# Kernel optimization log

Measured on AMD Instinct MI355X. Metric: run time of the kernel, lower is better.

The kernel has to match this reference:

```python
import jax, jax.numpy as jnp
import numpy as np

ALPHA = 0.2  # LeakyReLU negative slope
NEG = -9e15


def gat_layer(h, adj, W, a):
    # Faithful to the torch GAT: e_ij = leakyrelu(a^T [Wh_i || Wh_j])
    # = leakyrelu(a_src . Wh_i + a_dst . Wh_j); avoids the NxNx2F materialization.
    Wh = h @ W                              # [N, F]
    Fo = W.shape[1]
    a_src, a_dst = a[:Fo, 0], a[Fo:, 0]
    e = jax.nn.leaky_relu(
        (Wh @ a_src)[:, None] + (Wh @ a_dst)[None, :], negative_slope=ALPHA
    )                                        # [N, N]
    e = jnp.where(adj > 0, e, NEG)
    att = jax.nn.softmax(e, axis=1)          # dropout p=0 (eval)
    return jax.nn.elu(att @ Wh)


def gru_cell(x, h, W_ih, W_hh, b_ih, b_hh):
    # PyTorch GRUCell semantics.
    gi = x @ W_ih.T + b_ih                   # [N, 3F]
    gh = h @ W_hh.T + b_hh
    i_r, i_z, i_n = jnp.split(gi, 3, axis=1)
    h_r, h_z, h_n = jnp.split(gh, 3, axis=1)
    r = jax.nn.sigmoid(i_r + h_r)
    z = jax.nn.sigmoid(i_z + h_z)
    n = jnp.tanh(i_n + r * h_n)
    return (1.0 - z) * n + z * h


def setup_inputs() -> dict:
    key = jax.random.key(0)
    ks = jax.random.split(key, 10)
    N, nfeat, nhid, nout = 8192, 256, 128, 128
    x = jax.random.normal(ks[0], (N, nfeat), dtype=jnp.float32)
    # sparse random binary adjacency (~32 avg degree) + self loops
    adj = (jax.random.uniform(ks[1], (N, N)) < 0.004).astype(jnp.float32)
    adj = jnp.maximum(adj, jnp.eye(N, dtype=jnp.float32))
    h_prev = jnp.zeros((N, nout), dtype=jnp.float32)

    def xavier(k, shape, gain=1.414):
        fan_in, fan_out = shape[0], shape[1]
        b = gain * np.sqrt(6.0 / (fan_in + fan_out))
        return jax.random.uniform(k, shape, jnp.float32, -b, b)

    W1 = xavier(ks[2], (nfeat, nhid))
    a1 = xavier(ks[3], (2 * nhid, 1))
    W2 = xavier(ks[4], (nhid, nout))
    a2 = xavier(ks[5], (2 * nout, 1))
    s = 1.0 / np.sqrt(nout)
    W_ih = jax.random.uniform(ks[6], (3 * nout, nout), jnp.float32, -s, s)
    W_hh = jax.random.uniform(ks[7], (3 * nout, nout), jnp.float32, -s, s)
    b_ih = jax.random.uniform(ks[8], (3 * nout,), jnp.float32, -s, s)
    b_hh = jax.random.uniform(ks[9], (3 * nout,), jnp.float32, -s, s)
    return {"x": x, "adj": adj, "h_prev": h_prev, "W1": W1, "a1": a1,
            "W2": W2, "a2": a2, "W_ih": W_ih, "W_hh": W_hh,
            "b_ih": b_ih, "b_hh": b_hh}


def reference(x, adj, h_prev, W1, a1, W2, a2, W_ih, W_hh, b_ih, b_hh):
    x1 = gat_layer(x, adj, W1, a1)
    h_spat = gat_layer(x1, adj, W2, a2)
    return gru_cell(h_spat, h_prev, W_ih, W_hh, b_ih, b_hh)
```

## Files before the change

### kernel.cpp

```cpp
#include <hip/hip_runtime.h>
#include <math.h>

#define N_NODES 8192
#define CAP 128
#define LRELU_ALPHA 0.2f

typedef float v4f __attribute__((ext_vector_type(4)));

template <int K>
__device__ __forceinline__ void gemm_srcdst_body(
    int r0, int t, const float* __restrict__ A, const float* __restrict__ W,
    const float* __restrict__ a, float* __restrict__ Wh, float* __restrict__ src,
    float* __restrict__ dst, float* As, float (*red)[4][2]) {
  int c = t & 127, half = t >> 7;
  const float4* Ab4 = (const float4*)(A + (size_t)r0 * K);
  float4* As4 = (float4*)As;
#pragma unroll
  for (int l = t; l < 8 * K / 4; l += 256) As4[l] = Ab4[l];
  __syncthreads();
  float acc[4] = {0.f, 0.f, 0.f, 0.f};
  const float* Asl = As + (half * 4) * K;
#pragma unroll 8
  for (int k = 0; k < K; k++) {
    float wv = W[k * 128 + c];
#pragma unroll
    for (int r = 0; r < 4; r++) acc[r] += Asl[r * K + k] * wv;
  }
  float as = a[c], ad = a[128 + c];
  int wv_id = t >> 6, lane = t & 63;
#pragma unroll
  for (int r = 0; r < 4; r++) {
    int row = half * 4 + r;
    Wh[(size_t)(r0 + row) * 128 + c] = acc[r];
    float s = acc[r] * as, d = acc[r] * ad;
#pragma unroll
    for (int off = 32; off; off >>= 1) {
      s += __shfl_xor(s, off);
      d += __shfl_xor(d, off);
    }
    if (lane == 0) { red[wv_id][r][0] = s; red[wv_id][r][1] = d; }
  }
  __syncthreads();
  if (t < 8) {
    int wa = (t < 4) ? 0 : 2, rr = t & 3;
    src[r0 + t] = red[wa][rr][0] + red[wa + 1][rr][0];
    dst[r0 + t] = red[wa][rr][1] + red[wa + 1][rr][1];
  }
}

#define TR_B 64
__global__ __launch_bounds__(256) void gemm1_kernel(
    const float* __restrict__ x, const float* __restrict__ W1, const float* __restrict__ a1,
    float* __restrict__ Wh1, float* __restrict__ src1, float* __restrict__ dst1,
    const float* __restrict__ Wi, const float* __restrict__ Whm, float* __restrict__ WiT,
    float* __restrict__ WhT) {
  __shared__ float As[8 * 256];
  __shared__ float red[4][4][2];
  int t = threadIdx.x, bid = blockIdx.x;
  if (bid < 1024) {
    gemm_srcdst_body<256>(bid * 8, t, x, W1, a1, Wh1, src1, dst1, As, red);
  } else {
    for (int n = (bid - 1024) * 256 + t; n < 384 * 128; n += TR_B * 256) {
      int r = n >> 7, c = n & 127;
      WiT[c * 384 + r] = Wi[n];
      WhT[c * 384 + r] = Whm[n];
    }
  }
}

__global__ __launch_bounds__(256) void scan_agg_kernel(
    const float* __restrict__ adj, const float* __restrict__ Wh, const float* __restrict__ src,
    const float* __restrict__ dst, int* __restrict__ idx, int* __restrict__ counts,
    float* __restrict__ outp) {
  __shared__ int jn[CAP];
  __shared__ float w[CAP];
  __shared__ float redm[4];
  __shared__ float reds[4];
  __shared__ float accs[128];
  __shared__ int cnt;
  int i = blockIdx.x, t = threadIdx.x, lane = t & 63, wv = t >> 6;
  if (t == 0) cnt = 0;
  __syncthreads();
  const v4f* row = (const v4f*)(adj + (size_t)i * N_NODES);
  v4f v[8];
#pragma unroll
  for (int u = 0; u < 8; u++) v[u] = __builtin_nontemporal_load(row + t + 256 * u);
#pragma unroll
  for (int u = 0; u < 8; u++) {
    int n = (v[u].x > 0.f) + (v[u].y > 0.f) + (v[u].z > 0.f) + (v[u].w > 0.f);
    if (n) {
      int p = atomicAdd(&cnt, n);
      int j0 = (t + 256 * u) * 4;
      if (v[u].x > 0.f) { if (p < CAP) jn[p] = j0;     p++; }
      if (v[u].y > 0.f) { if (p < CAP) jn[p] = j0 + 1; p++; }
      if (v[u].z > 0.f) { if (p < CAP) jn[p] = j0 + 2; p++; }
      if (v[u].w > 0.f) { if (p < CAP) jn[p] = j0 + 3; p++; }
    }
  }
  __syncthreads();
  int c = cnt > CAP ? CAP : cnt;
  if (t < c) idx[(size_t)i * CAP + t] = jn[t];
  if (t == 0) counts[i] = c;
  float si = src[i];
  float e = -1e30f;
  if (t < c) {
    float x = si + dst[jn[t]];
    e = x > 0.f ? x : LRELU_ALPHA * x;
  }
  float m = e;
#pragma unroll
  for (int off = 32; off; off >>= 1) m = fmaxf(m, __shfl_xor(m, off));
  if (lane == 0) redm[wv] = m;
  __syncthreads();
  float M = fmaxf(fmaxf(redm[0], redm[1]), fmaxf(redm[2], redm[3]));
  float ex = 0.f;
  if (t < c) {
    ex = expf(e - M);
    w[t] = ex;
  }
  float s = ex;
#pragma unroll
  for (int off = 32; off; off >>= 1) s += __shfl_xor(s, off);
  if (lane == 0) reds[wv] = s;
  __syncthreads();
  float inv = 1.f / (reds[0] + reds[1] + reds[2] + reds[3]);
  int col = t & 127, half = t >> 7;
  float acc = 0.f;
  int k = half;
  for (; k + 2 < c; k += 4) {
    acc += w[k] * Wh[(size_t)jn[k] * 128 + col] + w[k + 2] * Wh[(size_t)jn[k + 2] * 128 + col];
  }
  for (; k < c; k += 2) acc += w[k] * Wh[(size_t)jn[k] * 128 + col];
  if (half == 0) accs[col] = acc;
  __syncthreads();
  if (half == 1) {
    float a = (accs[col] + acc) * inv;
    outp[(size_t)i * 128 + col] = a > 0.f ? a : expf(a) - 1.f;
  }
}

__global__ __launch_bounds__(256) void agg2_kernel(
    const float* __restrict__ Wh, const float* __restrict__ src, const float* __restrict__ dst,
    const int* __restrict__ idx, const int* __restrict__ counts, float* __restrict__ outp) {
  __shared__ int jn[CAP];
  __shared__ float w[CAP];
  __shared__ float redm[4];
  __shared__ float reds[4];
  __shared__ float accs[128];
  int i = blockIdx.x, t = threadIdx.x, lane = t & 63, wv = t >> 6;
  int c = counts[i];
  float si = src[i];
  float e = -1e30f;
  if (t < c) {
    int j = idx[(size_t)i * CAP + t];
    jn[t] = j;
    float x = si + dst[j];
    e = x > 0.f ? x : LRELU_ALPHA * x;
  }
  float m = e;
#pragma unroll
  for (int off = 32; off; off >>= 1) m = fmaxf(m, __shfl_xor(m, off));
  if (lane == 0) redm[wv] = m;
  __syncthreads();
  float M = fmaxf(fmaxf(redm[0], redm[1]), fmaxf(redm[2], redm[3]));
  float ex = 0.f;
  if (t < c) {
    ex = expf(e - M);
    w[t] = ex;
  }
  float s = ex;
#pragma unroll
  for (int off = 32; off; off >>= 1) s += __shfl_xor(s, off);
  if (lane == 0) reds[wv] = s;
  __syncthreads();
  float inv = 1.f / (reds[0] + reds[1] + reds[2] + reds[3]);
  int col = t & 127, half = t >> 7;
  float acc = 0.f;
  int k = half;
  for (; k + 2 < c; k += 4) {
    acc += w[k] * Wh[(size_t)jn[k] * 128 + col] + w[k + 2] * Wh[(size_t)jn[k + 2] * 128 + col];
  }
  for (; k < c; k += 2) acc += w[k] * Wh[(size_t)jn[k] * 128 + col];
  if (half == 0) accs[col] = acc;
  __syncthreads();
  if (half == 1) {
    float a = (accs[col] + acc) * inv;
    outp[(size_t)i * 128 + col] = a > 0.f ? a : expf(a) - 1.f;
  }
}

__global__ __launch_bounds__(256) void gemm_srcdst2_kernel(
    const float* __restrict__ A, const float* __restrict__ W, const float* __restrict__ a,
    float* __restrict__ Wh, float* __restrict__ src, float* __restrict__ dst) {
  __shared__ float As[8 * 128];
  __shared__ float red[4][4][2];
  gemm_srcdst_body<128>(blockIdx.x * 8, threadIdx.x, A, W, a, Wh, src, dst, As, red);
}

__global__ __launch_bounds__(256) void gru_kernel(
    const float* __restrict__ x, const float* __restrict__ h, const float* __restrict__ WiT,
    const float* __restrict__ WhT, const float* __restrict__ b_ih,
    const float* __restrict__ b_hh, float* __restrict__ outp) {
  __shared__ float xs[8 * 128];
  __shared__ float hs[8 * 128];
  int t = threadIdx.x, c = t & 127, half = t >> 7;
  int r0 = blockIdx.x * 8;
  {
    const float4* xb = (const float4*)(x + (size_t)r0 * 128);
    const float4* hb = (const float4*)(h + (size_t)r0 * 128);
    ((float4*)xs)[t] = xb[t];
    ((float4*)hs)[t] = hb[t];
  }
  __syncthreads();
  const float* xsl = xs + half * 4 * 128;
  const float* hsl = hs + half * 4 * 128;
  float rg[4], zg[4];
  {
    float ai[4] = {0.f}, ah[4] = {0.f};
#pragma unroll 4
    for (int k = 0; k < 128; k++) {
      float wi = WiT[k * 384 + c];
      float wh = WhT[k * 384 + c];
#pragma unroll
      for (int r = 0; r < 4; r++) {
        ai[r] += xsl[r * 128 + k] * wi;
        ah[r] += hsl[r * 128 + k] * wh;
      }
    }
    float bi = b_ih[c], bh = b_hh[c];
#pragma unroll
    for (int r = 0; r < 4; r++) rg[r] = 1.f / (1.f + expf(-(ai[r] + bi + ah[r] + bh)));
  }
  {
    float ai[4] = {0.f}, ah[4] = {0.f};
#pragma unroll 4
    for (int k = 0; k < 128; k++) {
      float wi = WiT[k * 384 + 128 + c];
      float wh = WhT[k * 384 + 128 + c];
#pragma unroll
      for (int r = 0; r < 4; r++) {
        ai[r] += xsl[r * 128 + k] * wi;
        ah[r] += hsl[r * 128 + k] * wh;
      }
    }
    float bi = b_ih[128 + c], bh = b_hh[128 + c];
#pragma unroll
    for (int r = 0; r < 4; r++) zg[r] = 1.f / (1.f + expf(-(ai[r] + bi + ah[r] + bh)));
  }
  {
    float ai[4] = {0.f}, ah[4] = {0.f};
#pragma unroll 4
    for (int k = 0; k < 128; k++) {
      float wi = WiT[k * 384 + 256 + c];
      float wh = WhT[k * 384 + 256 + c];
#pragma unroll
      for (int r = 0; r < 4; r++) {
        ai[r] += xsl[r * 128 + k] * wi;
        ah[r] += hsl[r * 128 + k] * wh;
      }
    }
    float bi = b_ih[256 + c], bh = b_hh[256 + c];
#pragma unroll
    for (int r = 0; r < 4; r++) {
      float n = tanhf(ai[r] + bi + rg[r] * (ah[r] + bh));
      float o = (1.f - zg[r]) * n + zg[r] * hsl[r * 128 + c];
      outp[(size_t)(r0 + half * 4 + r) * 128 + c] = o;
    }
  }
}

extern "C" void kernel_launch(void* const* d_in, const int* in_sizes, int n_in,
                              void* d_out, int out_size, void* d_ws, size_t ws_size,
                              hipStream_t stream) {
  const float* x     = (const float*)d_in[0];
  const float* adj   = (const float*)d_in[1];
  const float* hprev = (const float*)d_in[2];
  const float* W1    = (const float*)d_in[3];
  const float* a1    = (const float*)d_in[4];
  const float* W2    = (const float*)d_in[5];
  const float* a2    = (const float*)d_in[6];
  const float* W_ih  = (const float*)d_in[7];
  const float* W_hh  = (const float*)d_in[8];
  const float* b_ih  = (const float*)d_in[9];
  const float* b_hh  = (const float*)d_in[10];
  float* outp = (float*)d_out;

  char* p = (char*)d_ws;
  float* Wh1    = (float*)p; p += (size_t)N_NODES * 128 * 4;
  float* Wh2    = (float*)p; p += (size_t)N_NODES * 128 * 4;
  float* x1     = (float*)p; p += (size_t)N_NODES * 128 * 4;
  float* h_spat = (float*)p; p += (size_t)N_NODES * 128 * 4;
  float* src1   = (float*)p; p += (size_t)N_NODES * 4;
  float* dst1   = (float*)p; p += (size_t)N_NODES * 4;
  float* src2   = (float*)p; p += (size_t)N_NODES * 4;
  float* dst2   = (float*)p; p += (size_t)N_NODES * 4;
  float* WiT    = (float*)p; p += (size_t)384 * 128 * 4;
  float* WhT    = (float*)p; p += (size_t)384 * 128 * 4;
  int*   counts = (int*)p;   p += (size_t)N_NODES * 4;
  int*   idxbuf = (int*)p;   p += (size_t)N_NODES * CAP * 4;

  gemm1_kernel<<<1024 + TR_B, 256, 0, stream>>>(x, W1, a1, Wh1, src1, dst1, W_ih, W_hh, WiT, WhT);
  scan_agg_kernel<<<N_NODES, 256, 0, stream>>>(adj, Wh1, src1, dst1, idxbuf, counts, x1);
  gemm_srcdst2_kernel<<<N_NODES / 8, 256, 0, stream>>>(x1, W2, a2, Wh2, src2, dst2);
  agg2_kernel<<<N_NODES, 256, 0, stream>>>(Wh2, src2, dst2, idxbuf, counts, h_spat);
  gru_kernel<<<N_NODES / 8, 256, 0, stream>>>(h_spat, hprev, WiT, WhT, b_ih, b_hh, outp);
}
```

Baseline: 512.9 us.

## Fuse all stages into one cooperative persistent kernel with grid syncs

Replaces five separate launches with a single cooperative persistent kernel that runs every stage in grid-stride loops separated by grid.sync. Odd blocks scan adjacency rows first while even blocks run the first GEMM first, so the memory-bound adjacency scan overlaps with compute. Splitting the scan from the first aggregation means the gathered neighbour indices are written to and then reread from global memory. The change removes launch gaps and tail effects, but adds grid-wide barriers and limits the grid to resident occupancy, which can reduce latency hiding in the gather-heavy phases.

```diff
diff --git a/kernel.cpp b/kernel.cpp
--- a/kernel.cpp
+++ b/kernel.cpp
@@ -1,5 +1,8 @@
 #include <hip/hip_runtime.h>
+#include <hip/hip_cooperative_groups.h>
 #include <math.h>
+
+namespace cg = cooperative_groups;
 
 #define N_NODES 8192
 #define CAP 128
@@ -46,40 +49,13 @@
     src[r0 + t] = red[wa][rr][0] + red[wa + 1][rr][0];
     dst[r0 + t] = red[wa][rr][1] + red[wa + 1][rr][1];
   }
-}
-
-#define TR_B 64
-__global__ __launch_bounds__(256) void gemm1_kernel(
-    const float* __restrict__ x, const float* __restrict__ W1, const float* __restrict__ a1,
-    float* __restrict__ Wh1, float* __restrict__ src1, float* __restrict__ dst1,
-    const float* __restrict__ Wi, const float* __restrict__ Whm, float* __restrict__ WiT,
-    float* __restrict__ WhT) {
-  __shared__ float As[8 * 256];
-  __shared__ float red[4][4][2];
-  int t = threadIdx.x, bid = blockIdx.x;
-  if (bid < 1024) {
-    gemm_srcdst_body<256>(bid * 8, t, x, W1, a1, Wh1, src1, dst1, As, red);
-  } else {
-    for (int n = (bid - 1024) * 256 + t; n < 384 * 128; n += TR_B * 256) {
-      int r = n >> 7, c = n & 127;
-      WiT[c * 384 + r] = Wi[n];
-      WhT[c * 384 + r] = Whm[n];
-    }
-  }
-}
-
-__global__ __launch_bounds__(256) void scan_agg_kernel(
-    const float* __restrict__ adj, const float* __restrict__ Wh, const float* __restrict__ src,
-    const float* __restrict__ dst, int* __restrict__ idx, int* __restrict__ counts,
-    float* __restrict__ outp) {
-  __shared__ int jn[CAP];
-  __shared__ float w[CAP];
-  __shared__ float redm[4];
-  __shared__ float reds[4];
-  __shared__ float accs[128];
-  __shared__ int cnt;
-  int i = blockIdx.x, t = threadIdx.x, lane = t & 63, wv = t >> 6;
-  if (t == 0) cnt = 0;
+  __syncthreads();
+}
+
+__device__ __forceinline__ void scan_row(int i, int t, const float* __restrict__ adj,
+                                         int* __restrict__ idxbuf, int* __restrict__ counts,
+                                         int* jn, int* cntp) {
+  if (t == 0) *cntp = 0;
   __syncthreads();
   const v4f* row = (const v4f*)(adj + (size_t)i * N_NODES);
   v4f v[8];
@@ -89,7 +65,7 @@
   for (int u = 0; u < 8; u++) {
     int n = (v[u].x > 0.f) + (v[u].y > 0.f) + (v[u].z > 0.f) + (v[u].w > 0.f);
     if (n) {
-      int p = atomicAdd(&cnt, n);
+      int p = atomicAdd(cntp, n);
       int j0 = (t + 256 * u) * 4;
       if (v[u].x > 0.f) { if (p < CAP) jn[p] = j0;     p++; }
       if (v[u].y > 0.f) { if (p < CAP) jn[p] = j0 + 1; p++; }
@@ -98,13 +74,28 @@
     }
   }
   __syncthreads();
-  int c = cnt > CAP ? CAP : cnt;
-  if (t < c) idx[(size_t)i * CAP + t] = jn[t];
+  int c = *cntp;
+  if (c > CAP) c = CAP;
+  if (t < c) idxbuf[(size_t)i * CAP + t] = jn[t];
   if (t == 0) counts[i] = c;
+  __syncthreads();
+}
+
+__device__ __forceinline__ void agg_body(int i, int t, const float* __restrict__ Wh,
+                                         const float* __restrict__ src,
+                                         const float* __restrict__ dst,
+                                         const int* __restrict__ idxbuf,
+                                         const int* __restrict__ counts,
+                                         float* __restrict__ outp, int* jn, float* w,
+                                         float* redm, float* reds, float* accs) {
+  int lane = t & 63, wv = t >> 6;
+  int c = counts[i];
   float si = src[i];
   float e = -1e30f;
   if (t < c) {
-    float x = si + dst[jn[t]];
+    int j = idxbuf[(size_t)i * CAP + t];
+    jn[t] = j;
+    float x = si + dst[j];
     e = x > 0.f ? x : LRELU_ALPHA * x;
   }
   float m = e;
@@ -127,9 +118,8 @@
   int col = t & 127, half = t >> 7;
   float acc = 0.f;
   int k = half;
-  for (; k + 2 < c; k += 4) {
+  for (; k + 2 < c; k += 4)
     acc += w[k] * Wh[(size_t)jn[k] * 128 + col] + w[k + 2] * Wh[(size_t)jn[k + 2] * 128 + col];
-  }
   for (; k < c; k += 2) acc += w[k] * Wh[(size_t)jn[k] * 128 + col];
   if (half == 0) accs[col] = acc;
   __syncthreads();
@@ -137,80 +127,19 @@
     float a = (accs[col] + acc) * inv;
     outp[(size_t)i * 128 + col] = a > 0.f ? a : expf(a) - 1.f;
   }
-}
-
-__global__ __launch_bounds__(256) void agg2_kernel(
-    const float* __restrict__ Wh, const float* __restrict__ src, const float* __restrict__ dst,
-    const int* __restrict__ idx, const int* __restrict__ counts, float* __restrict__ outp) {
-  __shared__ int jn[CAP];
-  __shared__ float w[CAP];
-  __shared__ float redm[4];
-  __shared__ float reds[4];
-  __shared__ float accs[128];
-  int i = blockIdx.x, t = threadIdx.x, lane = t & 63, wv = t >> 6;
-  int c = counts[i];
-  float si = src[i];
-  float e = -1e30f;
-  if (t < c) {
-    int j = idx[(size_t)i * CAP + t];
-    jn[t] = j;
-    float x = si + dst[j];
-    e = x > 0.f ? x : LRELU_ALPHA * x;
-  }
-  float m = e;
-#pragma unroll
-  for (int off = 32; off; off >>= 1) m = fmaxf(m, __shfl_xor(m, off));
-  if (lane == 0) redm[wv] = m;
-  __syncthreads();
-  float M = fmaxf(fmaxf(redm[0], redm[1]), fmaxf(redm[2], redm[3]));
-  float ex = 0.f;
-  if (t < c) {
-    ex = expf(e - M);
-    w[t] = ex;
-  }
-  float s = ex;
-#pragma unroll
-  for (int off = 32; off; off >>= 1) s += __shfl_xor(s, off);
-  if (lane == 0) reds[wv] = s;
-  __syncthreads();
-  float inv = 1.f / (reds[0] + reds[1] + reds[2] + reds[3]);
-  int col = t & 127, half = t >> 7;
-  float acc = 0.f;
-  int k = half;
-  for (; k + 2 < c; k += 4) {
-    acc += w[k] * Wh[(size_t)jn[k] * 128 + col] + w[k + 2] * Wh[(size_t)jn[k + 2] * 128 + col];
-  }
-  for (; k < c; k += 2) acc += w[k] * Wh[(size_t)jn[k] * 128 + col];
-  if (half == 0) accs[col] = acc;
-  __syncthreads();
-  if (half == 1) {
-    float a = (accs[col] + acc) * inv;
-    outp[(size_t)i * 128 + col] = a > 0.f ? a : expf(a) - 1.f;
-  }
-}
-
-__global__ __launch_bounds__(256) void gemm_srcdst2_kernel(
-    const float* __restrict__ A, const float* __restrict__ W, const float* __restrict__ a,
-    float* __restrict__ Wh, float* __restrict__ src, float* __restrict__ dst) {
-  __shared__ float As[8 * 128];
-  __shared__ float red[4][4][2];
-  gemm_srcdst_body<128>(blockIdx.x * 8, threadIdx.x, A, W, a, Wh, src, dst, As, red);
-}
-
-__global__ __launch_bounds__(256) void gru_kernel(
-    const float* __restrict__ x, const float* __restrict__ h, const float* __restrict__ WiT,
-    const float* __restrict__ WhT, const float* __restrict__ b_ih,
-    const float* __restrict__ b_hh, float* __restrict__ outp) {
-  __shared__ float xs[8 * 128];
-  __shared__ float hs[8 * 128];
-  int t = threadIdx.x, c = t & 127, half = t >> 7;
-  int r0 = blockIdx.x * 8;
-  {
-    const float4* xb = (const float4*)(x + (size_t)r0 * 128);
-    const float4* hb = (const float4*)(h + (size_t)r0 * 128);
-    ((float4*)xs)[t] = xb[t];
-    ((float4*)hs)[t] = hb[t];
-  }
+  __syncthreads();
+}
+
+__device__ __forceinline__ void gru_body(int r0, int t, const float* __restrict__ x,
+                                         const float* __restrict__ h,
+                                         const float* __restrict__ WiT,
+                                         const float* __restrict__ WhT,
+                                         const float* __restrict__ b_ih,
+                                         const float* __restrict__ b_hh,
+                                         float* __restrict__ outp, float* xs, float* hs) {
+  int c = t & 127, half = t >> 7;
+  ((float4*)xs)[t] = ((const float4*)(x + (size_t)r0 * 128))[t];
+  ((float4*)hs)[t] = ((const float4*)(h + (size_t)r0 * 128))[t];
   __syncthreads();
   const float* xsl = xs + half * 4 * 128;
   const float* hsl = hs + half * 4 * 128;
@@ -219,13 +148,9 @@
     float ai[4] = {0.f}, ah[4] = {0.f};
 #pragma unroll 4
     for (int k = 0; k < 128; k++) {
-      float wi = WiT[k * 384 + c];
-      float wh = WhT[k * 384 + c];
-#pragma unroll
-      for (int r = 0; r < 4; r++) {
-        ai[r] += xsl[r * 128 + k] * wi;
-        ah[r] += hsl[r * 128 + k] * wh;
-      }
+      float wi = WiT[k * 384 + c], wh = WhT[k * 384 + c];
+#pragma unroll
+      for (int r = 0; r < 4; r++) { ai[r] += xsl[r * 128 + k] * wi; ah[r] += hsl[r * 128 + k] * wh; }
     }
     float bi = b_ih[c], bh = b_hh[c];
 #pragma unroll
@@ -235,13 +160,9 @@
     float ai[4] = {0.f}, ah[4] = {0.f};
 #pragma unroll 4
     for (int k = 0; k < 128; k++) {
-      float wi = WiT[k * 384 + 128 + c];
-      float wh = WhT[k * 384 + 128 + c];
-#pragma unroll
-      for (int r = 0; r < 4; r++) {
-        ai[r] += xsl[r * 128 + k] * wi;
-        ah[r] += hsl[r * 128 + k] * wh;
-      }
+      float wi = WiT[k * 384 + 128 + c], wh = WhT[k * 384 + 128 + c];
+#pragma unroll
+      for (int r = 0; r < 4; r++) { ai[r] += xsl[r * 128 + k] * wi; ah[r] += hsl[r * 128 + k] * wh; }
     }
     float bi = b_ih[128 + c], bh = b_hh[128 + c];
 #pragma unroll
@@ -251,22 +172,80 @@
     float ai[4] = {0.f}, ah[4] = {0.f};
 #pragma unroll 4
     for (int k = 0; k < 128; k++) {
-      float wi = WiT[k * 384 + 256 + c];
-      float wh = WhT[k * 384 + 256 + c];
-#pragma unroll
-      for (int r = 0; r < 4; r++) {
-        ai[r] += xsl[r * 128 + k] * wi;
-        ah[r] += hsl[r * 128 + k] * wh;
-      }
+      float wi = WiT[k * 384 + 256 + c], wh = WhT[k * 384 + 256 + c];
+#pragma unroll
+      for (int r = 0; r < 4; r++) { ai[r] += xsl[r * 128 + k] * wi; ah[r] += hsl[r * 128 + k] * wh; }
     }
     float bi = b_ih[256 + c], bh = b_hh[256 + c];
 #pragma unroll
     for (int r = 0; r < 4; r++) {
       float n = tanhf(ai[r] + bi + rg[r] * (ah[r] + bh));
-      float o = (1.f - zg[r]) * n + zg[r] * hsl[r * 128 + c];
-      outp[(size_t)(r0 + half * 4 + r) * 128 + c] = o;
-    }
-  }
+      outp[(size_t)(r0 + half * 4 + r) * 128 + c] =
+          (1.f - zg[r]) * n + zg[r] * hsl[r * 128 + c];
+    }
+  }
+  __syncthreads();
+}
+
+__global__ __launch_bounds__(256, 4) void mega_kernel(
+    const float* __restrict__ x, const float* __restrict__ adj, const float* __restrict__ hprev,
+    const float* __restrict__ W1, const float* __restrict__ a1, const float* __restrict__ W2,
+    const float* __restrict__ a2, const float* __restrict__ Wi, const float* __restrict__ Whm,
+    const float* __restrict__ b_ih, const float* __restrict__ b_hh, float* __restrict__ outp,
+    float* __restrict__ Wh1, float* __restrict__ Wh2, float* __restrict__ x1,
+    float* __restrict__ h_spat, float* __restrict__ src1, float* __restrict__ dst1,
+    float* __restrict__ src2, float* __restrict__ dst2, float* __restrict__ WiT,
+    float* __restrict__ WhT, int* __restrict__ counts, int* __restrict__ idxbuf, int NB) {
+  cg::grid_group grid = cg::this_grid();
+  __shared__ float As[8 * 256];
+  __shared__ float red[4][4][2];
+  __shared__ int jn[CAP];
+  __shared__ float w[CAP];
+  __shared__ float redm[4];
+  __shared__ float reds[4];
+  __shared__ float accs[128];
+  __shared__ int cnt;
+  int b = blockIdx.x, t = threadIdx.x;
+
+  if (b & 1) {
+    for (int i = b; i < N_NODES; i += NB) scan_row(i, t, adj, idxbuf, counts, jn, &cnt);
+    for (int n = b * 256 + t; n < 384 * 128; n += NB * 256) {
+      int r = n >> 7, c = n & 127;
+      WiT[c * 384 + r] = Wi[n];
+      WhT[c * 384 + r] = Whm[n];
+    }
+    for (int tile = b; tile < 1024; tile += NB)
+      gemm_srcdst_body<256>(tile * 8, t, x, W1, a1, Wh1, src1, dst1, As, red);
+  } else {
+    for (int n = b * 256 + t; n < 384 * 128; n += NB * 256) {
+      int r = n >> 7, c = n & 127;
+      WiT[c * 384 + r] = Wi[n];
+      WhT[c * 384 + r] = Whm[n];
+    }
+    for (int tile = b; tile < 1024; tile += NB)
+      gemm_srcdst_body<256>(tile * 8, t, x, W1, a1, Wh1, src1, dst1, As, red);
+    for (int i = b; i < N_NODES; i += NB) scan_row(i, t, adj, idxbuf, counts, jn, &cnt);
+  }
+  __threadfence();
+  grid.sync();
+
+  for (int i = b; i < N_NODES; i += NB)
+    agg_body(i, t, Wh1, src1, dst1, idxbuf, counts, x1, jn, w, redm, reds, accs);
+  __threadfence();
+  grid.sync();
+
+  for (int tile = b; tile < 1024; tile += NB)
+    gemm_srcdst_body<128>(tile * 8, t, x1, W2, a2, Wh2, src2, dst2, As, red);
+  __threadfence();
+  grid.sync();
+
+  for (int i = b; i < N_NODES; i += NB)
+    agg_body(i, t, Wh2, src2, dst2, idxbuf, counts, h_spat, jn, w, redm, reds, accs);
+  __threadfence();
+  grid.sync();
+
+  for (int tile = b; tile < 1024; tile += NB)
+    gru_body(tile * 8, t, h_spat, hprev, WiT, WhT, b_ih, b_hh, outp, As, As + 1024);
 }
 
 extern "C" void kernel_launch(void* const* d_in, const int* in_sizes, int n_in,
@@ -279,8 +258,8 @@
   const float* a1    = (const float*)d_in[4];
   const float* W2    = (const float*)d_in[5];
   const float* a2    = (const float*)d_in[6];
-  const float* W_ih  = (const float*)d_in[7];
-  const float* W_hh  = (const float*)d_in[8];
+  const float* Wi    = (const float*)d_in[7];
+  const float* Whm   = (const float*)d_in[8];
   const float* b_ih  = (const float*)d_in[9];
   const float* b_hh  = (const float*)d_in[10];
   float* outp = (float*)d_out;
@@ -299,9 +278,18 @@
   int*   counts = (int*)p;   p += (size_t)N_NODES * 4;
   int*   idxbuf = (int*)p;   p += (size_t)N_NODES * CAP * 4;
 
-  gemm1_kernel<<<1024 + TR_B, 256, 0, stream>>>(x, W1, a1, Wh1, src1, dst1, W_ih, W_hh, WiT, WhT);
-  scan_agg_kernel<<<N_NODES, 256, 0, stream>>>(adj, Wh1, src1, dst1, idxbuf, counts, x1);
-  gemm_srcdst2_kernel<<<N_NODES / 8, 256, 0, stream>>>(x1, W2, a2, Wh2, src2, dst2);
-  agg2_kernel<<<N_NODES, 256, 0, stream>>>(Wh2, src2, dst2, idxbuf, counts, h_spat);
-  gru_kernel<<<N_NODES / 8, 256, 0, stream>>>(h_spat, hprev, WiT, WhT, b_ih, b_hh, outp);
-}
+  int maxb = 0;
+  if (hipOccupancyMaxActiveBlocksPerMultiprocessor(
+          &maxb, reinterpret_cast<const void*>(mega_kernel), 256, 0) != hipSuccess ||
+      maxb < 1)
+    maxb = 2;
+  int nb = maxb * 256;
+  if (nb > 1024) nb = 1024;
+
+  void* args[] = {(void*)&x,     (void*)&adj,   (void*)&hprev, (void*)&W1,   (void*)&a1,
+                  (void*)&W2,    (void*)&a2,    (void*)&Wi,    (void*)&Whm,  (void*)&b_ih,
+                  (void*)&b_hh,  (void*)&outp,  (void*)&Wh1,   (void*)&Wh2,  (void*)&x1,
+                  (void*)&h_spat,(void*)&src1,  (void*)&dst1,  (void*)&src2, (void*)&dst2,
+                  (void*)&WiT,   (void*)&WhT,   (void*)&counts,(void*)&idxbuf,(void*)&nb};
+  hipLaunchCooperativeKernel((const void*)mega_kernel, dim3(nb), dim3(256), args, 0, stream);
+}
```

Result: slower. 1.023 ms (+99.4%).
